# Kernel tuning notes

Measured on AMD Instinct MI355X. Metric: run time of the kernel, lower is better.

## Reference

```python
import jax, jax.numpy as jnp
import numpy as np


def setup_inputs() -> dict:
    key = jax.random.key(0)
    kq, kk, kv = jax.random.split(key, 3)
    B, S, D = 4, 4096, 128
    q = jax.random.normal(kq, (B, S, D), dtype=jnp.float32)
    k = jax.random.normal(kk, (B, S, D), dtype=jnp.float32)
    v = jax.random.normal(kv, (B, S, D), dtype=jnp.float32)
    return {"q_proj": q, "k_proj": k, "v_proj": v}


def reference(q_proj, k_proj, v_proj):
    # FlashAttention's online-softmax tiling computes exactly standard
    # softmax attention: softmax(Q K^T / sqrt(d)) V (no mask, non-causal).
    d = q_proj.shape[-1]
    scale = 1.0 / jnp.sqrt(jnp.asarray(d, dtype=q_proj.dtype))
    logits = jnp.einsum('bqd,bkd->bqk', q_proj, k_proj) * scale
    probs = jax.nn.softmax(logits, axis=-1)  # numerically stable (max-subtracted)
    out = jnp.einsum('bqk,bkd->bqd', probs, v_proj)
    return out
```

## Files before the change

kernel.cpp:

```cpp
#include <hip/hip_runtime.h>

#define BATCH 4
#define SEQ   4096
#define DIM   128
#define BM    64
#define BN    64
#define NGROUP 2
#define TPG (SEQ / (BN * NGROUP))

#define QK_STRIDE 136
#define VT_STRIDE 72

typedef __attribute__((ext_vector_type(8))) __bf16 bf16x8;
typedef __attribute__((ext_vector_type(8))) unsigned short u16x8;
typedef __attribute__((ext_vector_type(4))) float f32x4;

__device__ __forceinline__ unsigned short f2bf(float f) {
    __bf16 h = (__bf16)f;
    return __builtin_bit_cast(unsigned short, h);
}

__device__ __forceinline__ bf16x8 lds_frag(const unsigned short* p) {
    u16x8 t = *(const u16x8*)p;
    return __builtin_bit_cast(bf16x8, t);
}

#define LDS_U16 (64 * QK_STRIDE + 128 * VT_STRIDE + 4 * 16 * VT_STRIDE)

extern "C" __global__ __launch_bounds__(256, 2)
void fa_part(const float* __restrict__ q, const float* __restrict__ k,
             const float* __restrict__ v, float* __restrict__ out,
             float* __restrict__ lsum)
{
    __shared__ __align__(16) unsigned short lds[LDS_U16];
    unsigned short* Ks = lds;
    unsigned short* Vt = lds + 64 * QK_STRIDE;

    const int tid  = threadIdx.x;
    const int wq   = tid >> 6;
    const int lane = tid & 63;
    const int l16  = lane & 15;
    const int quad = lane >> 4;

    unsigned short* Pw = Vt + 128 * VT_STRIDE + wq * 16 * VT_STRIDE;

    const int bid = blockIdx.x;
    const int xcd = bid & 7;
    const int g   = xcd & 1;
    const int b   = xcd >> 1;
    const int q0  = (bid >> 3) * BM;

    const float scale = 0.08838834764831845f;

    const float4* q4 = (const float4*)q;
    const float4* k4 = (const float4*)k;
    const float4* v4 = (const float4*)v;

    bf16x8 qfrag[4];
#pragma unroll
    for (int kc = 0; kc < 4; ++kc) {
        const float4* qp = &q4[(b * SEQ + q0 + wq * 16 + l16) * 32 + kc * 8 + quad * 2];
        float4 f0 = qp[0], f1 = qp[1];
        u16x8 u;
        u[0] = f2bf(f0.x * scale); u[1] = f2bf(f0.y * scale);
        u[2] = f2bf(f0.z * scale); u[3] = f2bf(f0.w * scale);
        u[4] = f2bf(f1.x * scale); u[5] = f2bf(f1.y * scale);
        u[6] = f2bf(f1.z * scale); u[7] = f2bf(f1.w * scale);
        qfrag[kc] = __builtin_bit_cast(bf16x8, u);
    }

    const int kv0 = g * (SEQ / NGROUP);

    float4 ldK[8], ldV[8];
#pragma unroll
    for (int i = 0; i < 8; ++i) {
        int idx = tid + i * 256;
        ldK[i] = k4[(b * SEQ + kv0 + (idx >> 5)) * 32 + (idx & 31)];
    }
#pragma unroll
    for (int i = 0; i < 8; ++i) {
        int idx = tid + i * 256;
        ldV[i] = v4[(b * SEQ + kv0 + (idx & 63)) * 32 + (idx >> 6)];
    }

    float l_part[4] = {0.f, 0.f, 0.f, 0.f};
    f32x4 accO[8];
#pragma unroll
    for (int ob = 0; ob < 8; ++ob) accO[ob] = (f32x4){0.f, 0.f, 0.f, 0.f};

    for (int t = 0; t < TPG; ++t) {
        __syncthreads();

#pragma unroll
        for (int i = 0; i < 8; ++i) {
            int idx = tid + i * 256;
            int row = idx >> 5, c4 = idx & 31;
            float4 f = ldK[i];
            ushort4 u;
            u.x = f2bf(f.x); u.y = f2bf(f.y); u.z = f2bf(f.z); u.w = f2bf(f.w);
            *(ushort4*)&Ks[row * QK_STRIDE + c4 * 4] = u;
        }
#pragma unroll
        for (int i = 0; i < 8; ++i) {
            int idx = tid + i * 256;
            int c4 = idx >> 6, key = idx & 63;
            float4 f = ldV[i];
            Vt[(c4 * 4 + 0) * VT_STRIDE + key] = f2bf(f.x);
            Vt[(c4 * 4 + 1) * VT_STRIDE + key] = f2bf(f.y);
            Vt[(c4 * 4 + 2) * VT_STRIDE + key] = f2bf(f.z);
            Vt[(c4 * 4 + 3) * VT_STRIDE + key] = f2bf(f.w);
        }
        __syncthreads();

        if (t + 1 < TPG) {
            const int kbase = kv0 + (t + 1) * BN;
#pragma unroll
            for (int i = 0; i < 8; ++i) {
                int idx = tid + i * 256;
                ldK[i] = k4[(b * SEQ + kbase + (idx >> 5)) * 32 + (idx & 31)];
            }
#pragma unroll
            for (int i = 0; i < 8; ++i) {
                int idx = tid + i * 256;
                ldV[i] = v4[(b * SEQ + kbase + (idx & 63)) * 32 + (idx >> 6)];
            }
        }

        f32x4 sfrag[4];
#pragma unroll
        for (int nb = 0; nb < 4; ++nb) sfrag[nb] = (f32x4){0.f, 0.f, 0.f, 0.f};
#pragma unroll
        for (int kc = 0; kc < 4; ++kc) {
            bf16x8 a = qfrag[kc];
#pragma unroll
            for (int nb = 0; nb < 4; ++nb) {
                bf16x8 bb = lds_frag(&Ks[(nb * 16 + l16) * QK_STRIDE + kc * 32 + quad * 8]);
                sfrag[nb] = __builtin_amdgcn_mfma_f32_16x16x32_bf16(a, bb, sfrag[nb], 0, 0, 0);
            }
        }

        __asm__ volatile("" ::: "memory");
#pragma unroll
        for (int nb = 0; nb < 4; ++nb)
#pragma unroll
            for (int r = 0; r < 4; ++r) {
                float pe = __expf(sfrag[nb][r]);
                l_part[r] += pe;
                Pw[(quad * 4 + r) * VT_STRIDE + nb * 16 + l16] = f2bf(pe);
            }
        __asm__ volatile("" ::: "memory");

#pragma unroll
        for (int kk = 0; kk < 2; ++kk) {
            bf16x8 a = lds_frag(&Pw[l16 * VT_STRIDE + kk * 32 + quad * 8]);
#pragma unroll
            for (int ob = 0; ob < 8; ++ob) {
                bf16x8 bb = lds_frag(&Vt[(ob * 16 + l16) * VT_STRIDE + kk * 32 + quad * 8]);
                accO[ob] = __builtin_amdgcn_mfma_f32_16x16x32_bf16(a, bb, accO[ob], 0, 0, 0);
            }
        }
    }

#pragma unroll
    for (int r = 0; r < 4; ++r) {
        float s = l_part[r];
        s += __shfl_xor(s, 1);
        s += __shfl_xor(s, 2);
        s += __shfl_xor(s, 4);
        s += __shfl_xor(s, 8);
        const int row = b * SEQ + q0 + wq * 16 + quad * 4 + r;
        if (l16 == 0) atomicAdd(&lsum[row], s);
        float* outp = out + (size_t)row * DIM;
#pragma unroll
        for (int ob = 0; ob < 8; ++ob)
            atomicAdd(&outp[ob * 16 + l16], accO[ob][r]);
    }
}

extern "C" __global__ void fa_norm(float* __restrict__ out, const float* __restrict__ lsum)
{
    int i = blockIdx.x * 256 + threadIdx.x;
    float inv = 1.0f / lsum[i >> 5];
    float4* o4 = (float4*)out;
    float4 vv = o4[i];
    vv.x *= inv; vv.y *= inv; vv.z *= inv; vv.w *= inv;
    o4[i] = vv;
}

extern "C" void kernel_launch(void* const* d_in, const int* in_sizes, int n_in,
                              void* d_out, int out_size, void* d_ws, size_t ws_size,
                              hipStream_t stream) {
    const float* q = (const float*)d_in[0];
    const float* k = (const float*)d_in[1];
    const float* v = (const float*)d_in[2];
    float* out  = (float*)d_out;
    float* lsum = (float*)d_ws;

    hipMemsetAsync(out,  0, (size_t)BATCH * SEQ * DIM * sizeof(float), stream);
    hipMemsetAsync(lsum, 0, (size_t)BATCH * SEQ * sizeof(float), stream);

    dim3 grid(BATCH * (SEQ / BM) * NGROUP);
    dim3 block(256);
    hipLaunchKernelGGL(fa_part, grid, block, 0, stream, q, k, v, out, lsum);

    dim3 ngrid((BATCH * SEQ * DIM / 4) / 256);
    hipLaunchKernelGGL(fa_norm, ngrid, block, 0, stream, out, lsum);
}
```

Before: 174.2 us.

## Swizzle LDS layouts, raise KV split to four groups, add MFMA priority hints

Drops the padded LDS strides and uses XOR swizzling on the K, V-transpose and P tiles to avoid bank conflicts with smaller shared memory. The KV sequence is split into four groups instead of two, doubling the grid and the atomic accumulation traffic into the output. Launch bounds now target four blocks per CU, and s_setprio raises wave priority around the MFMA loops. The extra split increases atomicAdd contention on the output and sum buffers, while shorter per-block loops and higher occupancy aim to improve latency hiding.

```diff
diff --git a/kernel.cpp b/kernel.cpp
--- a/kernel.cpp
+++ b/kernel.cpp
@@ -5,11 +5,12 @@
 #define DIM   128
 #define BM    64
 #define BN    64
-#define NGROUP 2
+#define NGROUP 4
 #define TPG (SEQ / (BN * NGROUP))
 
-#define QK_STRIDE 136
-#define VT_STRIDE 72
+#define KS_STRIDE 128
+#define VT_STRIDE 64
+#define PS_STRIDE 64
 
 typedef __attribute__((ext_vector_type(8))) __bf16 bf16x8;
 typedef __attribute__((ext_vector_type(8))) unsigned short u16x8;
@@ -25,16 +26,16 @@
     return __builtin_bit_cast(bf16x8, t);
 }
 
-#define LDS_U16 (64 * QK_STRIDE + 128 * VT_STRIDE + 4 * 16 * VT_STRIDE)
-
-extern "C" __global__ __launch_bounds__(256, 2)
+#define LDS_U16 (64 * KS_STRIDE + 128 * VT_STRIDE + 4 * 16 * PS_STRIDE)
+
+extern "C" __global__ __launch_bounds__(256, 4)
 void fa_part(const float* __restrict__ q, const float* __restrict__ k,
              const float* __restrict__ v, float* __restrict__ out,
              float* __restrict__ lsum)
 {
     __shared__ __align__(16) unsigned short lds[LDS_U16];
     unsigned short* Ks = lds;
-    unsigned short* Vt = lds + 64 * QK_STRIDE;
+    unsigned short* Vt = lds + 64 * KS_STRIDE;
 
     const int tid  = threadIdx.x;
     const int wq   = tid >> 6;
@@ -42,13 +43,13 @@
     const int l16  = lane & 15;
     const int quad = lane >> 4;
 
-    unsigned short* Pw = Vt + 128 * VT_STRIDE + wq * 16 * VT_STRIDE;
+    unsigned short* Pw = Vt + 128 * VT_STRIDE + wq * 16 * PS_STRIDE;
 
     const int bid = blockIdx.x;
-    const int xcd = bid & 7;
-    const int g   = xcd & 1;
-    const int b   = xcd >> 1;
-    const int q0  = (bid >> 3) * BM;
+    const int c   = bid & 15;
+    const int b   = c >> 2;
+    const int g   = c & 3;
+    const int q0  = (bid >> 4) * BM;
 
     const float scale = 0.08838834764831845f;
 
@@ -98,17 +99,18 @@
             float4 f = ldK[i];
             ushort4 u;
             u.x = f2bf(f.x); u.y = f2bf(f.y); u.z = f2bf(f.z); u.w = f2bf(f.w);
-            *(ushort4*)&Ks[row * QK_STRIDE + c4 * 4] = u;
+            *(ushort4*)&Ks[row * KS_STRIDE + ((c4 * 4) ^ (8 * (row & 7)))] = u;
         }
 #pragma unroll
         for (int i = 0; i < 8; ++i) {
             int idx = tid + i * 256;
             int c4 = idx >> 6, key = idx & 63;
             float4 f = ldV[i];
-            Vt[(c4 * 4 + 0) * VT_STRIDE + key] = f2bf(f.x);
-            Vt[(c4 * 4 + 1) * VT_STRIDE + key] = f2bf(f.y);
-            Vt[(c4 * 4 + 2) * VT_STRIDE + key] = f2bf(f.z);
-            Vt[(c4 * 4 + 3) * VT_STRIDE + key] = f2bf(f.w);
+            int r0 = c4 * 4;
+            Vt[(r0 + 0) * VT_STRIDE + (key ^ (8 * ((r0 + 0) & 7)))] = f2bf(f.x);
+            Vt[(r0 + 1) * VT_STRIDE + (key ^ (8 * ((r0 + 1) & 7)))] = f2bf(f.y);
+            Vt[(r0 + 2) * VT_STRIDE + (key ^ (8 * ((r0 + 2) & 7)))] = f2bf(f.z);
+            Vt[(r0 + 3) * VT_STRIDE + (key ^ (8 * ((r0 + 3) & 7)))] = f2bf(f.w);
         }
         __syncthreads();
 
@@ -129,15 +131,18 @@
         f32x4 sfrag[4];
 #pragma unroll
         for (int nb = 0; nb < 4; ++nb) sfrag[nb] = (f32x4){0.f, 0.f, 0.f, 0.f};
+        __builtin_amdgcn_s_setprio(1);
 #pragma unroll
         for (int kc = 0; kc < 4; ++kc) {
             bf16x8 a = qfrag[kc];
 #pragma unroll
             for (int nb = 0; nb < 4; ++nb) {
-                bf16x8 bb = lds_frag(&Ks[(nb * 16 + l16) * QK_STRIDE + kc * 32 + quad * 8]);
+                bf16x8 bb = lds_frag(&Ks[(nb * 16 + l16) * KS_STRIDE +
+                                         ((kc * 32 + quad * 8) ^ (8 * (l16 & 7)))]);
                 sfrag[nb] = __builtin_amdgcn_mfma_f32_16x16x32_bf16(a, bb, sfrag[nb], 0, 0, 0);
             }
         }
+        __builtin_amdgcn_s_setprio(0);
 
         __asm__ volatile("" ::: "memory");
 #pragma unroll
@@ -146,19 +151,24 @@
             for (int r = 0; r < 4; ++r) {
                 float pe = __expf(sfrag[nb][r]);
                 l_part[r] += pe;
-                Pw[(quad * 4 + r) * VT_STRIDE + nb * 16 + l16] = f2bf(pe);
+                int prow = quad * 4 + r;
+                Pw[prow * PS_STRIDE + ((nb * 16 + l16) ^ (8 * (prow & 7)))] = f2bf(pe);
             }
         __asm__ volatile("" ::: "memory");
 
+        __builtin_amdgcn_s_setprio(1);
 #pragma unroll
         for (int kk = 0; kk < 2; ++kk) {
-            bf16x8 a = lds_frag(&Pw[l16 * VT_STRIDE + kk * 32 + quad * 8]);
+            bf16x8 a = lds_frag(&Pw[l16 * PS_STRIDE +
+                                    ((kk * 32 + quad * 8) ^ (8 * (l16 & 7)))]);
 #pragma unroll
             for (int ob = 0; ob < 8; ++ob) {
-                bf16x8 bb = lds_frag(&Vt[(ob * 16 + l16) * VT_STRIDE + kk * 32 + quad * 8]);
+                bf16x8 bb = lds_frag(&Vt[(ob * 16 + l16) * VT_STRIDE +
+                                         ((kk * 32 + quad * 8) ^ (8 * (l16 & 7)))]);
                 accO[ob] = __builtin_amdgcn_mfma_f32_16x16x32_bf16(a, bb, accO[ob], 0, 0, 0);
             }
         }
+        __builtin_amdgcn_s_setprio(0);
     }
 
 #pragma unroll
@@ -204,5 +214,5 @@
     hipLaunchKernelGGL(fa_part, grid, block, 0, stream, q, k, v, out, lsum);
 
     dim3 ngrid((BATCH * SEQ * DIM / 4) / 256);
-    hipLaunchKernelGGL(fa_norm, ngrid, block, 0, stream, out, lsum);
-}
+    hipLaunchKernelGGL(fa_norm, ngrid, dim3(256), 0, stream, out, lsum);
+}
```

Result: slower. 505.8 us (+190.4%).
